# Kernel optimization log

Measured on AMD Instinct MI355X. Metric: run time of the kernel, lower is better.

## Reference

```python
import jax, jax.numpy as jnp
import numpy as np

B, N, C = 16, 2048, 256  # dim=256, hidden_dim=2*dim -> v,gate each width C
LN_EPS = 1e-5


def setup_inputs() -> dict:
    key = jax.random.key(0)
    ks = jax.random.split(key, 6)
    std = 0.02
    return {
        "x": jax.random.normal(ks[0], (B, N, C), dtype=jnp.float32),
        "H": 64,
        "W": 32,
        "ln_w": jnp.ones((C,), jnp.float32),
        "ln_b": jnp.zeros((C,), jnp.float32),
        "w_hidden": jax.random.normal(ks[1], (C, 2 * C), jnp.float32) * std,
        "b_hidden": jnp.zeros((2 * C,), jnp.float32),
        "w_kv": jax.random.normal(ks[2], (C, C), jnp.float32) * std,  # qkv_bias=False
        "gamma": jnp.ones((2, C), jnp.float32),   # torch.ones(2, dim)
        "beta": jnp.zeros((2, C), jnp.float32),   # torch.zeros(2, dim)
        "w_proj": jax.random.normal(ks[3], (C, C), jnp.float32) * std,
        "b_proj": jnp.zeros((C,), jnp.float32),
    }


def reference(x, H, W, ln_w, ln_b, w_hidden, b_hidden, w_kv, gamma, beta, w_proj, b_proj):
    # H, W are unused by the original forward (pos conv is dead code).
    b, n, c = x.shape
    # LayerNorm
    mu = jnp.mean(x, axis=-1, keepdims=True)
    var = jnp.mean(jnp.square(x - mu), axis=-1, keepdims=True)
    normed = (x - mu) * jax.lax.rsqrt(var + LN_EPS) * ln_w + ln_b
    # to_hidden: Linear + SiLU, then chunk into v, gate (each width c)
    h = jax.nn.silu(normed @ w_hidden + b_hidden)
    v, gate = h[..., :c], h[..., c:]
    # kv projection, then offset-scale into q, k
    Z = normed @ w_kv                                  # (b, n, c)
    QK = Z[..., None, :] * gamma + beta                # (b, n, 2, c)
    q, k = QK[..., 0, :], QK[..., 1, :]
    # relu^2 quadratic attention (no softmax)
    attn = jnp.einsum('bid,bjd->bij', q, k) / n        # (b, n, n)
    A = jnp.square(jax.nn.relu(attn))
    V = jnp.einsum('bij,bjd->bid', A, v)               # (b, n, c)
    # SiLU gating, output projection, residual
    out = (V * gate) @ w_proj + b_proj
    return out + x
```

## Files before the change

kernel.cpp:

```cpp
#include <hip/hip_runtime.h>

#define BN 32768
#define NB 16
#define NN 2048
#define CC 256
#define JT 64
#define NTILES (NN / JT)

using short8  = __attribute__((ext_vector_type(8))) short;
using floatx4 = __attribute__((ext_vector_type(4))) float;

__device__ __forceinline__ unsigned short f2bf(float f) {
  unsigned u = __builtin_bit_cast(unsigned, f);
  u += 0x7fffu + ((u >> 16) & 1u);
  return (unsigned short)(u >> 16);
}
__device__ __forceinline__ float bf2f(unsigned short h) {
  unsigned u = ((unsigned)h) << 16;
  return __builtin_bit_cast(float, u);
}
__device__ __forceinline__ unsigned pk4fp8(float a, float b, float c, float d) {
  unsigned u = __builtin_amdgcn_cvt_pk_fp8_f32(c, d, 0, true);
  return __builtin_amdgcn_cvt_pk_fp8_f32(a, b, (int)u, false);
}
__device__ __forceinline__ long lo64(uint4 v) {
  uint2 t; t.x = v.x; t.y = v.y; return __builtin_bit_cast(long, t);
}
__device__ __forceinline__ long hi64(uint4 v) {
  uint2 t; t.x = v.z; t.y = v.w; return __builtin_bit_cast(long, t);
}
__device__ __forceinline__ void gll16(const void* g, void* l) {
  __builtin_amdgcn_global_load_lds(
      (const __attribute__((address_space(1))) void*)g,
      (__attribute__((address_space(3))) void*)l, 16, 0, 0);
}
__device__ __forceinline__ float silu(float h) {
  return h / (1.0f + __expf(-h));
}

__global__ __launch_bounds__(256) void wconv_kernel(
    const float* __restrict__ wh, const float* __restrict__ wkv,
    const float* __restrict__ wp,
    unsigned short* __restrict__ wTh, unsigned short* __restrict__ wTkv,
    unsigned short* __restrict__ wTp) {
  __shared__ float T[64][65];
  int bid = blockIdx.x;
  const float* src; unsigned short* dst; int N, kt, nt;
  if (bid < 32)      { src = wh;  dst = wTh;  N = 512; kt = bid >> 3;        nt = bid & 7; }
  else if (bid < 48) { src = wkv; dst = wTkv; N = 256; kt = (bid - 32) >> 2; nt = (bid - 32) & 3; }
  else               { src = wp;  dst = wTp;  N = 256; kt = (bid - 48) >> 2; nt = (bid - 48) & 3; }
  int k0 = kt * 64, n0 = nt * 64;
  int t = threadIdx.x;
  int r = t >> 2, c0 = (t & 3) * 16;
#pragma unroll
  for (int e = 0; e < 4; ++e)
    *(float4*)(&T[r][c0 + e * 4]) =
        *(const float4*)(src + (size_t)(k0 + r) * N + n0 + c0 + e * 4);
  __syncthreads();
#pragma unroll
  for (int e = 0; e < 16; ++e)
    dst[(size_t)(n0 + r) * 256 + k0 + c0 + e] = f2bf(T[c0 + e][r]);
}

__global__ __launch_bounds__(256) void producer_kernel(
    const float* __restrict__ x, const float* __restrict__ lw,
    const float* __restrict__ lb,
    const unsigned short* __restrict__ wTh, const float* __restrict__ bh,
    const unsigned short* __restrict__ wTkv,
    const float* __restrict__ gamma, const float* __restrict__ beta,
    unsigned char* __restrict__ vB, unsigned short* __restrict__ gout,
    unsigned char* __restrict__ qout, unsigned char* __restrict__ kout) {
  __shared__ unsigned short Al[64 * 256];
  __shared__ unsigned char img[16384];
  const int t = threadIdx.x;
  const int mb = blockIdx.x * 64;
  {
    int r = t >> 2, q = t & 3;
    const float4* xp = (const float4*)(x + (size_t)(mb + r) * CC + q * 64);
    float4 xv[16];
#pragma unroll
    for (int f = 0; f < 16; ++f) xv[f] = xp[f];
    float s = 0.0f, s2 = 0.0f;
#pragma unroll
    for (int f = 0; f < 16; ++f) {
      s  += xv[f].x + xv[f].y + xv[f].z + xv[f].w;
      s2 += xv[f].x * xv[f].x + xv[f].y * xv[f].y
          + xv[f].z * xv[f].z + xv[f].w * xv[f].w;
    }
    s  += __shfl_xor(s, 1);  s  += __shfl_xor(s, 2);
    s2 += __shfl_xor(s2, 1); s2 += __shfl_xor(s2, 2);
    float mu = s * (1.0f / CC);
    float rs = rsqrtf(s2 * (1.0f / CC) - mu * mu + 1e-5f);
    const float4* lwp = (const float4*)(lw + q * 64);
    const float4* lbp = (const float4*)(lb + q * 64);
#pragma unroll
    for (int f = 0; f < 16; ++f) {
      float4 w = lwp[f], b = lbp[f];
      ushort4 o;
      o.x = f2bf((xv[f].x - mu) * rs * w.x + b.x);
      o.y = f2bf((xv[f].y - mu) * rs * w.y + b.y);
      o.z = f2bf((xv[f].z - mu) * rs * w.z + b.z);
      o.w = f2bf((xv[f].w - mu) * rs * w.w + b.w);
      int c16 = q * 8 + (f >> 1);
      *(ushort4*)((char*)Al + r * 512 + ((c16 ^ (r & 7)) * 16) + (f & 1) * 8) = o;
    }
  }
  __syncthreads();
  const int wave = t >> 6, lane = t & 63;
  const int m = lane & 15, g4 = lane >> 4;
  const int sw = (m >> 1) & 3;
  const int phys_base = g4;
  {
    floatx4 acc[4][4] = {};
#pragma unroll
    for (int ks = 0; ks < 8; ++ks) {
      short8 af[4], bf[4];
#pragma unroll
      for (int i = 0; i < 4; ++i)
        af[i] = *(const short8*)((const char*)Al + (i * 16 + m) * 512 +
                                 (((ks * 4 + phys_base) ^ (m & 7)) * 16));
#pragma unroll
      for (int j = 0; j < 4; ++j)
        bf[j] = *(const short8*)(wTh + (size_t)(wave * 64 + j * 16 + m) * 256 + ks * 32 + g4 * 8);
#pragma unroll
      for (int i = 0; i < 4; ++i)
#pragma unroll
        for (int j = 0; j < 4; ++j)
          acc[i][j] = __builtin_amdgcn_mfma_f32_16x16x32_bf16(af[i], bf[j], acc[i][j], 0, 0, 0);
    }
    const int jp4 = (g4 & 1) * 4;
    const int g4h = g4 >> 1;
#pragma unroll
    for (int j = 0; j < 4; ++j) {
      int col = wave * 64 + j * 16 + m;
      float bv = bh[col];
      int swc = (m >> 1) & 3;
#pragma unroll
      for (int i = 0; i < 4; ++i) {
        int g4a = ((i * 2 + g4h) & 3) ^ swc;
        int h8 = ((i >> 1) & 1) * 8;
        float s0 = silu(acc[i][j][0] + bv);
        float s1 = silu(acc[i][j][1] + bv);
        float s2 = silu(acc[i][j][2] + bv);
        float s3 = silu(acc[i][j][3] + bv);
        *(unsigned*)(img + col * 64 + g4a * 16 + h8 + jp4) = pk4fp8(s0, s1, s2, s3);
      }
    }
  }
  {
    floatx4 acc[4][4] = {};
#pragma unroll
    for (int ks = 0; ks < 8; ++ks) {
      short8 af[4], bf[4];
#pragma unroll
      for (int i = 0; i < 4; ++i)
        af[i] = *(const short8*)((const char*)Al + (i * 16 + m) * 512 +
                                 (((ks * 4 + phys_base) ^ (m & 7)) * 16));
#pragma unroll
      for (int j = 0; j < 4; ++j)
        bf[j] = *(const short8*)(wTh + (size_t)(256 + wave * 64 + j * 16 + m) * 256 + ks * 32 + g4 * 8);
#pragma unroll
      for (int i = 0; i < 4; ++i)
#pragma unroll
        for (int j = 0; j < 4; ++j)
          acc[i][j] = __builtin_amdgcn_mfma_f32_16x16x32_bf16(af[i], bf[j], acc[i][j], 0, 0, 0);
    }
#pragma unroll
    for (int j = 0; j < 4; ++j) {
      int colg = wave * 64 + j * 16 + m;
      float bv = bh[256 + colg];
#pragma unroll
      for (int i = 0; i < 4; ++i)
#pragma unroll
        for (int r = 0; r < 4; ++r) {
          int row = mb + i * 16 + g4 * 4 + r;
          gout[(size_t)row * CC + colg] = f2bf(silu(acc[i][j][r] + bv));
        }
    }
  }
  {
    floatx4 acc[4][4] = {};
#pragma unroll
    for (int ks = 0; ks < 8; ++ks) {
      short8 af[4], bf[4];
#pragma unroll
      for (int i = 0; i < 4; ++i)
        af[i] = *(const short8*)((const char*)Al + (i * 16 + m) * 512 +
                                 (((ks * 4 + phys_base) ^ (m & 7)) * 16));
#pragma unroll
      for (int j = 0; j < 4; ++j)
        bf[j] = *(const short8*)(wTkv + (size_t)(wave * 64 + j * 16 + m) * 256 + ks * 32 + g4 * 8);
#pragma unroll
      for (int i = 0; i < 4; ++i)
#pragma unroll
        for (int j = 0; j < 4; ++j)
          acc[i][j] = __builtin_amdgcn_mfma_f32_16x16x32_bf16(bf[j], af[i], acc[i][j], 0, 0, 0);
    }
#pragma unroll
    for (int j = 0; j < 4; ++j) {
      int c4 = wave * 64 + j * 16 + g4 * 4;
      float4 g0 = *(const float4*)(gamma + c4);
      float4 b0 = *(const float4*)(beta + c4);
      float4 g1 = *(const float4*)(gamma + CC + c4);
      float4 b1 = *(const float4*)(beta + CC + c4);
      int ks2 = c4 >> 6;
      int hsub = ((c4 >> 5) & 1) * 8 + (c4 & 7);
      int qsub = ((c4 >> 3) & 3) * 16 + hsub;
      int ksub = ((((c4 >> 3) & 3) ^ sw)) * 16 + hsub;
#pragma unroll
      for (int i = 0; i < 4; ++i) {
        int n = mb + i * 16 + m;
        int bb = n >> 11, jj = n & 2047;
        size_t base = (((size_t)bb * 128 + (jj >> 4)) * 4 + ks2) * 1024 + (size_t)m * 64;
        floatx4 z = acc[i][j];
        *(unsigned*)(qout + base + qsub) = pk4fp8(z[0] * g0.x + b0.x, z[1] * g0.y + b0.y,
                                                  z[2] * g0.z + b0.z, z[3] * g0.w + b0.w);
        *(unsigned*)(kout + base + ksub) = pk4fp8(z[0] * g1.x + b1.x, z[1] * g1.y + b1.y,
                                                  z[2] * g1.z + b1.z, z[3] * g1.w + b1.w);
      }
    }
  }
  __syncthreads();
  {
    const size_t tb = ((size_t)(mb >> 11) * 32 + ((mb & 2047) >> 6)) * 16384;
#pragma unroll
    for (int it = 0; it < 4; ++it) {
      int o = it * 4096 + t * 16;
      *(uint4*)(vB + tb + o) = *(const uint4*)(img + o);
    }
  }
}

__global__ __launch_bounds__(256, 2) void attn_kernel(
    const unsigned char* __restrict__ qB, const unsigned char* __restrict__ kB,
    const unsigned char* __restrict__ vB, const unsigned short* __restrict__ gg,
    unsigned short* __restrict__ og) {
  __shared__ unsigned char Kl[2][16384];
  __shared__ unsigned char Vl[2][16384];
  const int tid = threadIdx.x;
  const int wave = tid >> 6, lane = tid & 63;
  const int m = lane & 15, g4 = lane >> 4;
  const int id = blockIdx.x;
  const int b = id & 15, bx = id >> 4;
  const int i0 = bx * 64;
  const unsigned char* kimg = kB + (size_t)b * 524288;
  const unsigned char* vimg = vB + (size_t)b * 524288;

  const int iblk = bx * 4 + wave;
  uint4 qf[4];
#pragma unroll
  for (int ks2 = 0; ks2 < 4; ++ks2)
    qf[ks2] = *(const uint4*)(qB + ((size_t)(b * 128 + iblk) * 4 + ks2) * 1024 + m * 64 + g4 * 16);

  floatx4 acc[16] = {};
  const int alo = (m + ((g4 & 1) << 5)) << 2;
  const int ahi = alo + 64;
  const int gsw = (g4 ^ ((m >> 1) & 3)) * 16;

  auto stage = [&](int buf, int t) {
    const unsigned char* kt = kimg + (size_t)t * 16384;
    const unsigned char* vt = vimg + (size_t)t * 16384;
#pragma unroll
    for (int it = 0; it < 4; ++it) {
      int o = (it * 256 + tid) * 16;
      gll16(kt + o, &Kl[buf][o]);
      gll16(vt + o, &Vl[buf][o]);
    }
  };

  stage(0, 0);
  for (int t = 0; t < NTILES; ++t) {
    const int cur = t & 1;
    __syncthreads();
    if (t + 1 < NTILES) stage(cur ^ 1, t + 1);
    floatx4 sacc[4] = {};
#pragma unroll
    for (int ks2 = 0; ks2 < 4; ++ks2) {
#pragma unroll
      for (int jf = 0; jf < 4; ++jf) {
        uint4 kf = *(const uint4*)(&Kl[cur][(jf * 4 + ks2) * 1024 + m * 64 + gsw]);
        sacc[jf] = __builtin_amdgcn_mfma_f32_16x16x32_fp8_fp8(
            lo64(kf), lo64(qf[ks2]), sacc[jf], 0, 0, 0);
        sacc[jf] = __builtin_amdgcn_mfma_f32_16x16x32_fp8_fp8(
            hi64(kf), hi64(qf[ks2]), sacc[jf], 0, 0, 0);
      }
    }
    unsigned pk[4];
#pragma unroll
    for (int jf = 0; jf < 4; ++jf) {
      float p0 = fmaxf(sacc[jf][0], 0.0f) * 0.0625f;
      float p1 = fmaxf(sacc[jf][1], 0.0f) * 0.0625f;
      float p2 = fmaxf(sacc[jf][2], 0.0f) * 0.0625f;
      float p3 = fmaxf(sacc[jf][3], 0.0f) * 0.0625f;
      pk[jf] = pk4fp8(p0 * p0, p1 * p1, p2 * p2, p3 * p3);
    }
    long ap[2];
#pragma unroll
    for (int kk = 0; kk < 2; ++kk) {
      int A0 = __builtin_amdgcn_ds_bpermute(alo, (int)pk[2 * kk]);
      int B0 = __builtin_amdgcn_ds_bpermute(alo, (int)pk[2 * kk + 1]);
      int C0 = __builtin_amdgcn_ds_bpermute(ahi, (int)pk[2 * kk]);
      int D0 = __builtin_amdgcn_ds_bpermute(ahi, (int)pk[2 * kk + 1]);
      unsigned lo = (g4 & 2) ? (unsigned)B0 : (unsigned)A0;
      unsigned hi = (g4 & 2) ? (unsigned)D0 : (unsigned)C0;
      ap[kk] = (long)(((unsigned long long)hi << 32) | lo);
    }
#pragma unroll
    for (int cf = 0; cf < 16; ++cf) {
      uint4 vfr = *(const uint4*)(&Vl[cur][cf * 1024 + m * 64 + gsw]);
      acc[cf] = __builtin_amdgcn_mfma_f32_16x16x32_fp8_fp8(ap[0], lo64(vfr), acc[cf], 0, 0, 0);
      acc[cf] = __builtin_amdgcn_mfma_f32_16x16x32_fp8_fp8(ap[1], hi64(vfr), acc[cf], 0, 0, 0);
    }
  }
  const float sc = 1.0f / 16384.0f;
  const size_t bo = (size_t)b * NN * CC;
#pragma unroll
  for (int cf = 0; cf < 16; ++cf)
#pragma unroll
    for (int r = 0; r < 4; ++r) {
      int row = i0 + wave * 16 + g4 * 4 + r;
      int col = cf * 16 + m;
      size_t off = bo + (size_t)row * CC + col;
      og[off] = f2bf(acc[cf][r] * sc * bf2f(gg[off]));
    }
}

__global__ __launch_bounds__(256) void gemm_proj(
    const unsigned short* __restrict__ A, const unsigned short* __restrict__ BT,
    const float* __restrict__ bias, const float* __restrict__ xres,
    float* __restrict__ out) {
  int wave = threadIdx.x >> 6, lane = threadIdx.x & 63;
  int m = lane & 15, g4 = lane >> 4, kb = g4 * 8;
  int m0 = blockIdx.x * 128 + (wave & 1) * 64;
  int n0 = blockIdx.y * 128 + (wave >> 1) * 64;
  floatx4 acc[4][4] = {};
#pragma unroll
  for (int ks = 0; ks < 8; ++ks) {
    short8 af[4], bf[4];
#pragma unroll
    for (int i = 0; i < 4; ++i)
      af[i] = *(const short8*)(A + (size_t)(m0 + i * 16 + m) * CC + ks * 32 + kb);
#pragma unroll
    for (int j = 0; j < 4; ++j)
      bf[j] = *(const short8*)(BT + (size_t)(n0 + j * 16 + m) * CC + ks * 32 + kb);
#pragma unroll
    for (int i = 0; i < 4; ++i)
#pragma unroll
      for (int j = 0; j < 4; ++j)
        acc[i][j] = __builtin_amdgcn_mfma_f32_16x16x32_bf16(af[i], bf[j], acc[i][j], 0, 0, 0);
  }
#pragma unroll
  for (int j = 0; j < 4; ++j) {
    int col = n0 + j * 16 + m;
    float bv = bias[col];
#pragma unroll
    for (int i = 0; i < 4; ++i)
#pragma unroll
      for (int r = 0; r < 4; ++r) {
        int row = m0 + i * 16 + g4 * 4 + r;
        size_t rr = (size_t)row * CC;
        out[rr + col] = acc[i][j][r] + bv + xres[rr + col];
      }
  }
}

extern "C" void kernel_launch(void* const* d_in, const int* in_sizes, int n_in,
                              void* d_out, int out_size, void* d_ws, size_t ws_size,
                              hipStream_t stream) {
  const float* x        = (const float*)d_in[0];
  const float* ln_w     = (const float*)d_in[3];
  const float* ln_b     = (const float*)d_in[4];
  const float* w_hidden = (const float*)d_in[5];
  const float* b_hidden = (const float*)d_in[6];
  const float* w_kv     = (const float*)d_in[7];
  const float* gamma    = (const float*)d_in[8];
  const float* beta     = (const float*)d_in[9];
  const float* w_proj   = (const float*)d_in[10];
  const float* b_proj   = (const float*)d_in[11];
  float* out = (float*)d_out;
  char* ws = (char*)d_ws;

  const size_t SZ = (size_t)BN * CC * 2;
  const size_t HZ = SZ / 2;
  unsigned short* slot0 = (unsigned short*)(ws);
  unsigned short* gbuf  = (unsigned short*)(ws + SZ);
  unsigned char*  qB    = (unsigned char*)(ws + 2 * SZ);
  unsigned char*  kB    = (unsigned char*)(ws + 2 * SZ + HZ);
  unsigned char*  vB    = (unsigned char*)(ws + 2 * SZ + 2 * HZ);
  unsigned short* wTh   = (unsigned short*)(ws + 2 * SZ + 3 * HZ);
  unsigned short* wTkv  = (unsigned short*)(ws + 2 * SZ + 3 * HZ + 512 * 256 * 2);
  unsigned short* wTp   = (unsigned short*)(ws + 2 * SZ + 3 * HZ + 512 * 256 * 2 + 256 * 256 * 2);

  wconv_kernel<<<64, 256, 0, stream>>>(w_hidden, w_kv, w_proj, wTh, wTkv, wTp);
  producer_kernel<<<BN / 64, 256, 0, stream>>>(
      x, ln_w, ln_b, wTh, b_hidden, wTkv, gamma, beta, vB, gbuf, qB, kB);
  attn_kernel<<<512, 256, 0, stream>>>(qB, kB, vB, gbuf, slot0);
  gemm_proj<<<dim3(BN / 128, 2), 256, 0, stream>>>(slot0, wTp, b_proj, x, out);
}
```

Baseline: 150.7 us.

## Split producer kernel into three blocks per row tile, one per projection

The producer grid triples, so each 64-row tile gets three blocks. Each block recomputes LayerNorm and then runs only one of the three GEMMs (v, gate, or q/k). The v output is now written straight to global memory in the tiled layout instead of being staged through a 16KB shared image, and x is reloaded in the normalize pass instead of held in registers. This aims to raise parallelism and occupancy, using less shared memory and fewer registers, at the cost of redundant LayerNorm and reading x three times.

```diff
diff --git a/kernel.cpp b/kernel.cpp
--- a/kernel.cpp
+++ b/kernel.cpp
@@ -71,21 +71,19 @@
     unsigned char* __restrict__ vB, unsigned short* __restrict__ gout,
     unsigned char* __restrict__ qout, unsigned char* __restrict__ kout) {
   __shared__ unsigned short Al[64 * 256];
-  __shared__ unsigned char img[16384];
   const int t = threadIdx.x;
-  const int mb = blockIdx.x * 64;
+  const int id = blockIdx.x;
+  const int pass = id % 3;
+  const int mb = (id / 3) * 64;
   {
     int r = t >> 2, q = t & 3;
     const float4* xp = (const float4*)(x + (size_t)(mb + r) * CC + q * 64);
-    float4 xv[16];
-#pragma unroll
-    for (int f = 0; f < 16; ++f) xv[f] = xp[f];
     float s = 0.0f, s2 = 0.0f;
 #pragma unroll
     for (int f = 0; f < 16; ++f) {
-      s  += xv[f].x + xv[f].y + xv[f].z + xv[f].w;
-      s2 += xv[f].x * xv[f].x + xv[f].y * xv[f].y
-          + xv[f].z * xv[f].z + xv[f].w * xv[f].w;
+      float4 v = xp[f];
+      s  += v.x + v.y + v.z + v.w;
+      s2 += v.x * v.x + v.y * v.y + v.z * v.z + v.w * v.w;
     }
     s  += __shfl_xor(s, 1);  s  += __shfl_xor(s, 2);
     s2 += __shfl_xor(s2, 1); s2 += __shfl_xor(s2, 2);
@@ -93,14 +91,16 @@
     float rs = rsqrtf(s2 * (1.0f / CC) - mu * mu + 1e-5f);
     const float4* lwp = (const float4*)(lw + q * 64);
     const float4* lbp = (const float4*)(lb + q * 64);
+    asm volatile("" ::: "memory");
 #pragma unroll
     for (int f = 0; f < 16; ++f) {
+      float4 v = xp[f];
       float4 w = lwp[f], b = lbp[f];
       ushort4 o;
-      o.x = f2bf((xv[f].x - mu) * rs * w.x + b.x);
-      o.y = f2bf((xv[f].y - mu) * rs * w.y + b.y);
-      o.z = f2bf((xv[f].z - mu) * rs * w.z + b.z);
-      o.w = f2bf((xv[f].w - mu) * rs * w.w + b.w);
+      o.x = f2bf((v.x - mu) * rs * w.x + b.x);
+      o.y = f2bf((v.y - mu) * rs * w.y + b.y);
+      o.z = f2bf((v.z - mu) * rs * w.z + b.z);
+      o.w = f2bf((v.w - mu) * rs * w.w + b.w);
       int c16 = q * 8 + (f >> 1);
       *(ushort4*)((char*)Al + r * 512 + ((c16 ^ (r & 7)) * 16) + (f & 1) * 8) = o;
     }
@@ -109,8 +109,7 @@
   const int wave = t >> 6, lane = t & 63;
   const int m = lane & 15, g4 = lane >> 4;
   const int sw = (m >> 1) & 3;
-  const int phys_base = g4;
-  {
+  if (pass == 0) {
     floatx4 acc[4][4] = {};
 #pragma unroll
     for (int ks = 0; ks < 8; ++ks) {
@@ -118,7 +117,7 @@
 #pragma unroll
       for (int i = 0; i < 4; ++i)
         af[i] = *(const short8*)((const char*)Al + (i * 16 + m) * 512 +
-                                 (((ks * 4 + phys_base) ^ (m & 7)) * 16));
+                                 (((ks * 4 + g4) ^ (m & 7)) * 16));
 #pragma unroll
       for (int j = 0; j < 4; ++j)
         bf[j] = *(const short8*)(wTh + (size_t)(wave * 64 + j * 16 + m) * 256 + ks * 32 + g4 * 8);
@@ -128,26 +127,26 @@
         for (int j = 0; j < 4; ++j)
           acc[i][j] = __builtin_amdgcn_mfma_f32_16x16x32_bf16(af[i], bf[j], acc[i][j], 0, 0, 0);
     }
+    const size_t tb = ((size_t)(mb >> 11) * 32 + ((mb & 2047) >> 6)) * 16384;
     const int jp4 = (g4 & 1) * 4;
     const int g4h = g4 >> 1;
 #pragma unroll
     for (int j = 0; j < 4; ++j) {
       int col = wave * 64 + j * 16 + m;
       float bv = bh[col];
-      int swc = (m >> 1) & 3;
+      size_t colb = tb + (size_t)col * 64;
 #pragma unroll
       for (int i = 0; i < 4; ++i) {
-        int g4a = ((i * 2 + g4h) & 3) ^ swc;
+        int g4a = ((i * 2 + g4h) & 3) ^ sw;
         int h8 = ((i >> 1) & 1) * 8;
         float s0 = silu(acc[i][j][0] + bv);
         float s1 = silu(acc[i][j][1] + bv);
         float s2 = silu(acc[i][j][2] + bv);
         float s3 = silu(acc[i][j][3] + bv);
-        *(unsigned*)(img + col * 64 + g4a * 16 + h8 + jp4) = pk4fp8(s0, s1, s2, s3);
+        *(unsigned*)(vB + colb + g4a * 16 + h8 + jp4) = pk4fp8(s0, s1, s2, s3);
       }
     }
-  }
-  {
+  } else if (pass == 1) {
     floatx4 acc[4][4] = {};
 #pragma unroll
     for (int ks = 0; ks < 8; ++ks) {
@@ -155,7 +154,7 @@
 #pragma unroll
       for (int i = 0; i < 4; ++i)
         af[i] = *(const short8*)((const char*)Al + (i * 16 + m) * 512 +
-                                 (((ks * 4 + phys_base) ^ (m & 7)) * 16));
+                                 (((ks * 4 + g4) ^ (m & 7)) * 16));
 #pragma unroll
       for (int j = 0; j < 4; ++j)
         bf[j] = *(const short8*)(wTh + (size_t)(256 + wave * 64 + j * 16 + m) * 256 + ks * 32 + g4 * 8);
@@ -177,8 +176,7 @@
           gout[(size_t)row * CC + colg] = f2bf(silu(acc[i][j][r] + bv));
         }
     }
-  }
-  {
+  } else {
     floatx4 acc[4][4] = {};
 #pragma unroll
     for (int ks = 0; ks < 8; ++ks) {
@@ -186,7 +184,7 @@
 #pragma unroll
       for (int i = 0; i < 4; ++i)
         af[i] = *(const short8*)((const char*)Al + (i * 16 + m) * 512 +
-                                 (((ks * 4 + phys_base) ^ (m & 7)) * 16));
+                                 (((ks * 4 + g4) ^ (m & 7)) * 16));
 #pragma unroll
       for (int j = 0; j < 4; ++j)
         bf[j] = *(const short8*)(wTkv + (size_t)(wave * 64 + j * 16 + m) * 256 + ks * 32 + g4 * 8);
@@ -218,15 +216,6 @@
         *(unsigned*)(kout + base + ksub) = pk4fp8(z[0] * g1.x + b1.x, z[1] * g1.y + b1.y,
                                                   z[2] * g1.z + b1.z, z[3] * g1.w + b1.w);
       }
-    }
-  }
-  __syncthreads();
-  {
-    const size_t tb = ((size_t)(mb >> 11) * 32 + ((mb & 2047) >> 6)) * 16384;
-#pragma unroll
-    for (int it = 0; it < 4; ++it) {
-      int o = it * 4096 + t * 16;
-      *(uint4*)(vB + tb + o) = *(const uint4*)(img + o);
     }
   }
 }
@@ -392,7 +381,7 @@
   unsigned short* wTp   = (unsigned short*)(ws + 2 * SZ + 3 * HZ + 512 * 256 * 2 + 256 * 256 * 2);
 
   wconv_kernel<<<64, 256, 0, stream>>>(w_hidden, w_kv, w_proj, wTh, wTkv, wTp);
-  producer_kernel<<<BN / 64, 256, 0, stream>>>(
+  producer_kernel<<<(BN / 64) * 3, 256, 0, stream>>>(
       x, ln_w, ln_b, wTh, b_hidden, wTkv, gamma, beta, vB, gbuf, qB, kB);
   attn_kernel<<<512, 256, 0, stream>>>(qB, kB, vB, gbuf, slot0);
   gemm_proj<<<dim3(BN / 128, 2), 256, 0, stream>>>(slot0, wTp, b_proj, x, out);
```

Result: slower. 177.2 us (+17.6%).
